# Performance work log

Hardware: AMD Instinct MI355X
Metric: run time of the kernel (lower is better)

Reference implementation:

```python
import jax, jax.numpy as jnp
import numpy as np

B, S, D_IN, D_OUT = 4, 2048, 4096, 4096
N_ADAPTERS, MAX_RANK = 8, 16


def setup_inputs() -> dict:
    key = jax.random.key(0)
    ks = jax.random.split(key, 7)
    x = jax.random.normal(ks[0], (B, S, D_IN), dtype=jnp.float32)
    weight = jax.random.normal(ks[1], (D_OUT, D_IN), dtype=jnp.float32) * (1.0 / np.sqrt(D_IN))
    bias = jax.random.normal(ks[2], (D_OUT,), dtype=jnp.float32) * 0.01
    lora_a_weights = jax.random.normal(ks[3], (N_ADAPTERS, MAX_RANK, D_IN), dtype=jnp.float32) * (1.0 / np.sqrt(D_IN))
    lora_b_weights = jax.random.normal(ks[4], (N_ADAPTERS, D_OUT, MAX_RANK), dtype=jnp.float32) * 0.02
    scaling_factors = jax.random.uniform(ks[5], (N_ADAPTERS,), dtype=jnp.float32, minval=0.5, maxval=2.0)
    adapter_id = jax.random.randint(ks[6], (B,), 0, N_ADAPTERS, dtype=jnp.int64)
    return {
        "x": x,
        "weight": weight,
        "bias": bias,
        "lora_a_weights": lora_a_weights,
        "lora_b_weights": lora_b_weights,
        "scaling_factors": scaling_factors,
        "adapter_id": adapter_id,
    }


def reference(x, weight, bias, lora_a_weights, lora_b_weights, scaling_factors, adapter_id):
    # Base linear: [B,S,Din] @ [Dout,Din]^T + bias -> [B,S,Dout]
    base = jnp.einsum('bsi,oi->bso', x, weight) + bias
    # Per-batch adapter gather (Punica/S-LoRA style bgmv)
    a_sel = lora_a_weights[adapter_id]      # [B, R, Din]
    b_sel = lora_b_weights[adapter_id]      # [B, Dout, R]
    scale = scaling_factors[adapter_id]     # [B]
    low = jnp.einsum('bsi,bri->bsr', x, a_sel)          # [B, S, R]
    delta = jnp.einsum('bsr,bor->bso', low, b_sel)      # [B, S, Dout]
    return base + scale[:, None, None] * delta
```

## Files before the change

kernel.cpp:

```cpp
#include <hip/hip_runtime.h>
#include <hip/hip_bf16.h>

#define BATCH 4
#define SEQ   2048
#define DIN   4096
#define DOUT  4096
#define MTOT  (BATCH * SEQ)
#define RANK  16

typedef __bf16 bf8_t  __attribute__((ext_vector_type(8)));
typedef float  f4_t   __attribute__((ext_vector_type(4)));

#define GLD_LDS(g, l) \
  __builtin_amdgcn_global_load_lds((const __attribute__((address_space(1))) void*)(g), \
                                   (__attribute__((address_space(3))) void*)(l), 16, 0, 0)

__global__ __launch_bounds__(256) void conv_kernel(
    const float* __restrict__ w, __bf16* __restrict__ wb) {
  const size_t i = ((size_t)blockIdx.x * 256 + threadIdx.x) * 8;
  f4_t a = *(const f4_t*)(w + i);
  f4_t b = *(const f4_t*)(w + i + 4);
  bf8_t o;
#pragma unroll
  for (int e = 0; e < 4; ++e) { o[e] = (__bf16)a[e]; o[4 + e] = (__bf16)b[e]; }
  *(bf8_t*)(wb + i) = o;
}

__global__ __launch_bounds__(256) void lora_low_kernel(
    const __bf16* __restrict__ xb, const float* __restrict__ Aw,
    const float* __restrict__ scales, const int* __restrict__ adapter_id,
    float* __restrict__ lowS) {
  const int t    = threadIdx.x;
  const int w    = t >> 6;
  const int lane = t & 63;
  const int quad = lane >> 4;
  const int l16  = lane & 15;
  const int m0   = blockIdx.x * 64;
  const int kb   = blockIdx.y * 512;
  const int b    = adapter_id[m0 >> 11];
  const float scale = scales[b];

  const int row = m0 + w * 16 + l16;
  const __bf16* xp = xb + (size_t)row * DIN + kb + quad * 8;
  const float*  ap = Aw + ((size_t)b * RANK + l16) * DIN + kb + quad * 8;

  f4_t acc = (f4_t)0.f;
#pragma unroll 4
  for (int it = 0; it < 16; ++it) {
    const int off = it * 32;
    bf8_t af = *(const bf8_t*)(xp + off);
    f4_t v0 = *(const f4_t*)(ap + off);
    f4_t v1 = *(const f4_t*)(ap + off + 4);
    bf8_t bfr;
#pragma unroll
    for (int e = 0; e < 4; ++e) { bfr[e] = (__bf16)v0[e]; bfr[4 + e] = (__bf16)v1[e]; }
    acc = __builtin_amdgcn_mfma_f32_16x16x32_bf16(af, bfr, acc, 0, 0, 0);
  }
#pragma unroll
  for (int e = 0; e < 4; ++e)
    atomicAdd(&lowS[(size_t)(m0 + w * 16 + quad * 4 + e) * RANK + l16], acc[e] * scale);
}

#define BM 256
#define BN 256
#define BKK 32
#define NT (DIN / BKK)

__global__ __launch_bounds__(512, 2) void lora_gemm_kernel(
    const __bf16* __restrict__ x, const __bf16* __restrict__ wgt,
    const float* __restrict__ bias, const float* __restrict__ loraB,
    const int* __restrict__ adapter_id, const float* __restrict__ lowS,
    float* __restrict__ out) {
  __shared__ __bf16 lds[4][2][BM * BKK];

  const int t    = threadIdx.x;
  const int w    = t >> 6;
  const int lane = t & 63;
  const int quad = lane >> 4;
  const int l16  = lane & 15;
  const int wm   = w >> 2;
  const int wn   = w & 3;
  const int m0 = blockIdx.y * BM;
  const int n0 = blockIdx.x * BN;

  const int sr = t >> 2;
  const int sc = (t & 3) ^ ((sr >> 1) & 3);
  const __bf16* gA = x   + (size_t)(m0 + sr) * DIN + sc * 8;
  const __bf16* gB = wgt + (size_t)(n0 + sr) * DIN + sc * 8;
  const int ldst = w * 512;

  const int fc   = (quad ^ ((l16 >> 1) & 3)) * 8;
  const int aoff = (wm * 128 + l16) * BKK + fc;
  const int boff = (wn * 64  + l16) * BKK + fc;

  f4_t acc[8][4];
#pragma unroll
  for (int i = 0; i < 8; ++i)
#pragma unroll
    for (int j = 0; j < 4; ++j) acc[i][j] = (f4_t)0.f;

#define STAGE(s, k0) do {                                      \
    GLD_LDS(gA + (k0),              &lds[s][0][ldst]);         \
    GLD_LDS(gA + (k0) + 128 * DIN,  &lds[s][0][4096 + ldst]);  \
    GLD_LDS(gB + (k0),              &lds[s][1][ldst]);         \
    GLD_LDS(gB + (k0) + 128 * DIN,  &lds[s][1][4096 + ldst]);  \
  } while (0)

  auto body = [&](int s) {
    bf8_t a[8], b[4];
#pragma unroll
    for (int mf = 0; mf < 8; ++mf)
      a[mf] = *(const bf8_t*)&lds[s][0][aoff + mf * (16 * BKK)];
#pragma unroll
    for (int nf = 0; nf < 4; ++nf)
      b[nf] = *(const bf8_t*)&lds[s][1][boff + nf * (16 * BKK)];
    __builtin_amdgcn_s_setprio(1);
#pragma unroll
    for (int mf = 0; mf < 8; ++mf)
#pragma unroll
      for (int nf = 0; nf < 4; ++nf)
        acc[mf][nf] = __builtin_amdgcn_mfma_f32_16x16x32_bf16(a[mf], b[nf], acc[mf][nf], 0, 0, 0);
    __builtin_amdgcn_s_setprio(0);
  };

  STAGE(0, 0); STAGE(1, BKK); STAGE(2, 2 * BKK);
  for (int it = 0; it < NT - 3; ++it) {
    STAGE((it + 3) & 3, (it + 3) * BKK);
    asm volatile("s_waitcnt vmcnt(12)" ::: "memory");
    __builtin_amdgcn_s_barrier();
    body(it & 3);
    __builtin_amdgcn_s_barrier();
  }
  asm volatile("s_waitcnt vmcnt(8)" ::: "memory");
  __builtin_amdgcn_s_barrier();
  body((NT - 3) & 3);
  __builtin_amdgcn_s_barrier();
  asm volatile("s_waitcnt vmcnt(4)" ::: "memory");
  __builtin_amdgcn_s_barrier();
  body((NT - 2) & 3);
  __builtin_amdgcn_s_barrier();
  asm volatile("s_waitcnt vmcnt(0)" ::: "memory");
  __builtin_amdgcn_s_barrier();
  body((NT - 1) & 3);
#undef STAGE

  const int b = adapter_id[m0 >> 11];
  bf8_t alow[8], blow[4];
  if (quad < 2) {
#pragma unroll
    for (int mf = 0; mf < 8; ++mf) {
      const float* p = &lowS[(size_t)(m0 + wm * 128 + mf * 16 + l16) * RANK + quad * 8];
      f4_t u0 = *(const f4_t*)p;
      f4_t u1 = *(const f4_t*)(p + 4);
#pragma unroll
      for (int e = 0; e < 4; ++e) { alow[mf][e] = (__bf16)u0[e]; alow[mf][4 + e] = (__bf16)u1[e]; }
    }
#pragma unroll
    for (int nf = 0; nf < 4; ++nf) {
      const float* p = &loraB[((size_t)b * DOUT + n0 + wn * 64 + nf * 16 + l16) * RANK + quad * 8];
      f4_t u0 = *(const f4_t*)p;
      f4_t u1 = *(const f4_t*)(p + 4);
#pragma unroll
      for (int e = 0; e < 4; ++e) { blow[nf][e] = (__bf16)u0[e]; blow[nf][4 + e] = (__bf16)u1[e]; }
    }
  } else {
#pragma unroll
    for (int i = 0; i < 8; ++i)
#pragma unroll
      for (int e = 0; e < 8; ++e) alow[i][e] = (__bf16)0.f;
#pragma unroll
    for (int j = 0; j < 4; ++j)
#pragma unroll
      for (int e = 0; e < 8; ++e) blow[j][e] = (__bf16)0.f;
  }
#pragma unroll
  for (int mf = 0; mf < 8; ++mf)
#pragma unroll
    for (int nf = 0; nf < 4; ++nf)
      acc[mf][nf] = __builtin_amdgcn_mfma_f32_16x16x32_bf16(alow[mf], blow[nf], acc[mf][nf], 0, 0, 0);

#pragma unroll
  for (int nf = 0; nf < 4; ++nf) {
    const int c = n0 + wn * 64 + nf * 16 + l16;
    const float bc = bias[c];
#pragma unroll
    for (int mf = 0; mf < 8; ++mf) {
      const int r0 = m0 + wm * 128 + mf * 16 + quad * 4;
#pragma unroll
      for (int e = 0; e < 4; ++e)
        out[(size_t)(r0 + e) * DOUT + c] = acc[mf][nf][e] + bc;
    }
  }
}

extern "C" void kernel_launch(void* const* d_in, const int* in_sizes, int n_in,
                              void* d_out, int out_size, void* d_ws, size_t ws_size,
                              hipStream_t stream) {
  const float* x       = (const float*)d_in[0];
  const float* weight  = (const float*)d_in[1];
  const float* bias    = (const float*)d_in[2];
  const float* lora_a  = (const float*)d_in[3];
  const float* lora_b  = (const float*)d_in[4];
  const float* scaling = (const float*)d_in[5];
  const int*   adapter = (const int*)d_in[6];
  float* out = (float*)d_out;

  __bf16* xb   = (__bf16*)d_ws;
  __bf16* wb   = xb + (size_t)MTOT * DIN;
  float*  lowS = (float*)(wb + (size_t)DOUT * DIN);

  hipMemsetAsync(lowS, 0, (size_t)MTOT * RANK * sizeof(float), stream);
  conv_kernel<<<(size_t)DOUT * DIN / 8 / 256, 256, 0, stream>>>(weight, wb);
  conv_kernel<<<(size_t)MTOT * DIN / 8 / 256, 256, 0, stream>>>(x, xb);
  dim3 lgrid(MTOT / 64, 8);
  lora_low_kernel<<<lgrid, 256, 0, stream>>>(xb, lora_a, scaling, adapter, lowS);
  dim3 grid(DOUT / BN, MTOT / BM);
  lora_gemm_kernel<<<grid, 512, 0, stream>>>(xb, wb, bias, lora_b, adapter, lowS, out);
}
```

Baseline: 557.4 us.

## Fuse x conversion into LoRA-down kernel and restructure GEMM pipeline with BK=64

```diff
diff --git a/kernel.cpp b/kernel.cpp
--- a/kernel.cpp
+++ b/kernel.cpp
@@ -15,7 +15,7 @@
   __builtin_amdgcn_global_load_lds((const __attribute__((address_space(1))) void*)(g), \
                                    (__attribute__((address_space(3))) void*)(l), 16, 0, 0)
 
-__global__ __launch_bounds__(256) void conv_kernel(
+__global__ __launch_bounds__(256) void conv_w_kernel(
     const float* __restrict__ w, __bf16* __restrict__ wb) {
   const size_t i = ((size_t)blockIdx.x * 256 + threadIdx.x) * 8;
   f4_t a = *(const f4_t*)(w + i);
@@ -27,9 +27,9 @@
 }
 
 __global__ __launch_bounds__(256) void lora_low_kernel(
-    const __bf16* __restrict__ xb, const float* __restrict__ Aw,
+    const float* __restrict__ x, const float* __restrict__ Aw,
     const float* __restrict__ scales, const int* __restrict__ adapter_id,
-    float* __restrict__ lowS) {
+    __bf16* __restrict__ xb, float* __restrict__ lowS) {
   const int t    = threadIdx.x;
   const int w    = t >> 6;
   const int lane = t & 63;
@@ -41,19 +41,25 @@
   const float scale = scales[b];
 
   const int row = m0 + w * 16 + l16;
-  const __bf16* xp = xb + (size_t)row * DIN + kb + quad * 8;
-  const float*  ap = Aw + ((size_t)b * RANK + l16) * DIN + kb + quad * 8;
+  const float*  xp  = x  + (size_t)row * DIN + kb + quad * 8;
+  __bf16*       xbp = xb + (size_t)row * DIN + kb + quad * 8;
+  const float*  ap  = Aw + ((size_t)b * RANK + l16) * DIN + kb + quad * 8;
 
   f4_t acc = (f4_t)0.f;
 #pragma unroll 4
   for (int it = 0; it < 16; ++it) {
     const int off = it * 32;
-    bf8_t af = *(const bf8_t*)(xp + off);
+    f4_t u0 = *(const f4_t*)(xp + off);
+    f4_t u1 = *(const f4_t*)(xp + off + 4);
     f4_t v0 = *(const f4_t*)(ap + off);
     f4_t v1 = *(const f4_t*)(ap + off + 4);
-    bf8_t bfr;
-#pragma unroll
-    for (int e = 0; e < 4; ++e) { bfr[e] = (__bf16)v0[e]; bfr[4 + e] = (__bf16)v1[e]; }
+    bf8_t af, bfr;
+#pragma unroll
+    for (int e = 0; e < 4; ++e) {
+      af[e] = (__bf16)u0[e]; af[4 + e] = (__bf16)u1[e];
+      bfr[e] = (__bf16)v0[e]; bfr[4 + e] = (__bf16)v1[e];
+    }
+    *(bf8_t*)(xbp + off) = af;
     acc = __builtin_amdgcn_mfma_f32_16x16x32_bf16(af, bfr, acc, 0, 0, 0);
   }
 #pragma unroll
@@ -63,15 +69,19 @@
 
 #define BM 256
 #define BN 256
-#define BKK 32
-#define NT (DIN / BKK)
+#define BKT 64
+#define NT (DIN / BKT)
+#define NIT (NT / 2)
+
+#define BAR() __builtin_amdgcn_s_barrier()
+#define VMW(n) asm volatile("s_waitcnt vmcnt(" #n ")" ::: "memory")
 
 __global__ __launch_bounds__(512, 2) void lora_gemm_kernel(
     const __bf16* __restrict__ x, const __bf16* __restrict__ wgt,
     const float* __restrict__ bias, const float* __restrict__ loraB,
     const int* __restrict__ adapter_id, const float* __restrict__ lowS,
     float* __restrict__ out) {
-  __shared__ __bf16 lds[4][2][BM * BKK];
+  __shared__ __bf16 lds[2][2][2][128 * 64];
 
   const int t    = threadIdx.x;
   const int w    = t >> 6;
@@ -80,71 +90,103 @@
   const int l16  = lane & 15;
   const int wm   = w >> 2;
   const int wn   = w & 3;
-  const int m0 = blockIdx.y * BM;
-  const int n0 = blockIdx.x * BN;
-
-  const int sr = t >> 2;
-  const int sc = (t & 3) ^ ((sr >> 1) & 3);
-  const __bf16* gA = x   + (size_t)(m0 + sr) * DIN + sc * 8;
-  const __bf16* gB = wgt + (size_t)(n0 + sr) * DIN + sc * 8;
-  const int ldst = w * 512;
-
-  const int fc   = (quad ^ ((l16 >> 1) & 3)) * 8;
-  const int aoff = (wm * 128 + l16) * BKK + fc;
-  const int boff = (wn * 64  + l16) * BKK + fc;
-
+
+  const int linear = blockIdx.y * 16 + blockIdx.x;
+  const int swz = (linear & 7) * 64 + (linear >> 3);
+  const int m0 = (swz >> 4) * BM;
+  const int n0 = (swz & 15) * BN;
+
+  const int srow = t >> 3;
+  const int sc   = (t & 7) ^ ((t >> 4) & 7);
+  const __bf16* gA = x   + (size_t)(m0 + srow) * DIN + sc * 8;
+  const __bf16* gB = wgt + (size_t)(n0 + srow) * DIN + sc * 8;
+  const int ldsw = w * 512;
+
+#define STG(buf, mat, half, kel, gp) do {                                        \
+    GLD_LDS((gp) + (size_t)((half) * 128) * DIN + (kel),                         \
+            &lds[buf][mat][half][ldsw]);                                         \
+    GLD_LDS((gp) + (size_t)((half) * 128 + 64) * DIN + (kel),                    \
+            &lds[buf][mat][half][4096 + ldsw]);                                  \
+  } while (0)
+
+  const int st0 = (quad ^ ((l16 >> 1) & 7)) * 8;
+  const int st1 = ((4 + quad) ^ ((l16 >> 1) & 7)) * 8;
+
+  bf8_t a[4][2], b[2][2];
   f4_t acc[8][4];
 #pragma unroll
   for (int i = 0; i < 8; ++i)
 #pragma unroll
     for (int j = 0; j < 4; ++j) acc[i][j] = (f4_t)0.f;
 
-#define STAGE(s, k0) do {                                      \
-    GLD_LDS(gA + (k0),              &lds[s][0][ldst]);         \
-    GLD_LDS(gA + (k0) + 128 * DIN,  &lds[s][0][4096 + ldst]);  \
-    GLD_LDS(gB + (k0),              &lds[s][1][ldst]);         \
-    GLD_LDS(gB + (k0) + 128 * DIN,  &lds[s][1][4096 + ldst]);  \
-  } while (0)
-
-  auto body = [&](int s) {
-    bf8_t a[8], b[4];
-#pragma unroll
-    for (int mf = 0; mf < 8; ++mf)
-      a[mf] = *(const bf8_t*)&lds[s][0][aoff + mf * (16 * BKK)];
-#pragma unroll
-    for (int nf = 0; nf < 4; ++nf)
-      b[nf] = *(const bf8_t*)&lds[s][1][boff + nf * (16 * BKK)];
-    __builtin_amdgcn_s_setprio(1);
-#pragma unroll
-    for (int mf = 0; mf < 8; ++mf)
-#pragma unroll
-      for (int nf = 0; nf < 4; ++nf)
-        acc[mf][nf] = __builtin_amdgcn_mfma_f32_16x16x32_bf16(a[mf], b[nf], acc[mf][nf], 0, 0, 0);
-    __builtin_amdgcn_s_setprio(0);
-  };
-
-  STAGE(0, 0); STAGE(1, BKK); STAGE(2, 2 * BKK);
-  for (int it = 0; it < NT - 3; ++it) {
-    STAGE((it + 3) & 3, (it + 3) * BKK);
-    asm volatile("s_waitcnt vmcnt(12)" ::: "memory");
-    __builtin_amdgcn_s_barrier();
-    body(it & 3);
-    __builtin_amdgcn_s_barrier();
-  }
-  asm volatile("s_waitcnt vmcnt(8)" ::: "memory");
-  __builtin_amdgcn_s_barrier();
-  body((NT - 3) & 3);
-  __builtin_amdgcn_s_barrier();
-  asm volatile("s_waitcnt vmcnt(4)" ::: "memory");
-  __builtin_amdgcn_s_barrier();
-  body((NT - 2) & 3);
-  __builtin_amdgcn_s_barrier();
-  asm volatile("s_waitcnt vmcnt(0)" ::: "memory");
-  __builtin_amdgcn_s_barrier();
-  body((NT - 1) & 3);
-#undef STAGE
-
-  const int b = adapter_id[m0 >> 11];
+#define LDA(buf, mh) do {                                                        \
+    const __bf16* base_ = &lds[buf][0][wm][0];                                   \
+    _Pragma("unroll")                                                            \
+    for (int mq = 0; mq < 4; ++mq) {                                             \
+      const int r_ = ((mh) * 4 + mq) * 16 + l16;                                 \
+      a[mq][0] = *(const bf8_t*)(base_ + r_ * 64 + st0);                         \
+      a[mq][1] = *(const bf8_t*)(base_ + r_ * 64 + st1);                         \
+    }                                                                            \
+  } while (0)
+
+#define LDB(buf, nh) do {                                                        \
+    const __bf16* base_ = &lds[buf][1][wn >> 1][(wn & 1) * 4096];                \
+    _Pragma("unroll")                                                            \
+    for (int nq = 0; nq < 2; ++nq) {                                             \
+      const int r_ = ((nh) * 2 + nq) * 16 + l16;                                 \
+      b[nq][0] = *(const bf8_t*)(base_ + r_ * 64 + st0);                         \
+      b[nq][1] = *(const bf8_t*)(base_ + r_ * 64 + st1);                         \
+    }                                                                            \
+  } while (0)
+
+#define MM(mh, nh) do {                                                          \
+    __builtin_amdgcn_s_setprio(1);                                               \
+    _Pragma("unroll")                                                            \
+    for (int ks = 0; ks < 2; ++ks)                                               \
+      _Pragma("unroll")                                                          \
+      for (int mq = 0; mq < 4; ++mq)                                             \
+        _Pragma("unroll")                                                        \
+        for (int nq = 0; nq < 2; ++nq)                                           \
+          acc[(mh) * 4 + mq][(nh) * 2 + nq] = __builtin_amdgcn_mfma_f32_16x16x32_bf16( \
+              a[mq][ks], b[nq][ks], acc[(mh) * 4 + mq][(nh) * 2 + nq], 0, 0, 0); \
+    __builtin_amdgcn_s_setprio(0);                                               \
+  } while (0)
+
+  STG(0, 0, 0, 0, gA); STG(0, 0, 1, 0, gA);
+  STG(0, 1, 0, 0, gB); STG(0, 1, 1, 0, gB);
+  STG(1, 0, 0, BKT, gA); STG(1, 1, 1, BKT, gB);
+  VMW(4);
+  BAR();
+
+  for (int it = 0; it < NIT; ++it) {
+    const int k1 = (2 * it + 1) * BKT;
+    const int k2 = ((2 * it + 2) & (NT - 1)) * BKT;
+    const int k3 = ((2 * it + 3) & (NT - 1)) * BKT;
+    LDA(0, 0); LDB(0, 0); STG(1, 1, 0, k1, gB);
+    BAR(); MM(0, 0); BAR();
+    LDB(0, 1); STG(1, 0, 1, k1, gA);
+    BAR(); MM(0, 1); BAR();
+    LDA(0, 1); STG(0, 0, 0, k2, gA);
+    BAR(); MM(1, 1); BAR();
+    LDB(0, 0); STG(0, 1, 1, k2, gB);
+    VMW(4);
+    BAR(); MM(1, 0); BAR();
+    LDA(1, 0); LDB(1, 0); STG(0, 1, 0, k2, gB);
+    BAR(); MM(0, 0); BAR();
+    LDB(1, 1); STG(0, 0, 1, k2, gA);
+    BAR(); MM(0, 1); BAR();
+    LDA(1, 1); STG(1, 0, 0, k3, gA);
+    BAR(); MM(1, 1); BAR();
+    LDB(1, 0); STG(1, 1, 1, k3, gB);
+    VMW(4);
+    BAR(); MM(1, 0); BAR();
+  }
+#undef STG
+#undef LDA
+#undef LDB
+#undef MM
+
+  const int b_id = adapter_id[m0 >> 11];
   bf8_t alow[8], blow[4];
   if (quad < 2) {
 #pragma unroll
@@ -157,7 +199,7 @@
     }
 #pragma unroll
     for (int nf = 0; nf < 4; ++nf) {
-      const float* p = &loraB[((size_t)b * DOUT + n0 + wn * 64 + nf * 16 + l16) * RANK + quad * 8];
+      const float* p = &loraB[((size_t)b_id * DOUT + n0 + wn * 64 + nf * 16 + l16) * RANK + quad * 8];
       f4_t u0 = *(const f4_t*)p;
       f4_t u1 = *(const f4_t*)(p + 4);
 #pragma unroll
@@ -210,10 +252,9 @@
   float*  lowS = (float*)(wb + (size_t)DOUT * DIN);
 
   hipMemsetAsync(lowS, 0, (size_t)MTOT * RANK * sizeof(float), stream);
-  conv_kernel<<<(size_t)DOUT * DIN / 8 / 256, 256, 0, stream>>>(weight, wb);
-  conv_kernel<<<(size_t)MTOT * DIN / 8 / 256, 256, 0, stream>>>(x, xb);
+  conv_w_kernel<<<(size_t)DOUT * DIN / 8 / 256, 256, 0, stream>>>(weight, wb);
   dim3 lgrid(MTOT / 64, 8);
-  lora_low_kernel<<<lgrid, 256, 0, stream>>>(xb, lora_a, scaling, adapter, lowS);
+  lora_low_kernel<<<lgrid, 256, 0, stream>>>(x, lora_a, scaling, adapter, xb, lowS);
   dim3 grid(DOUT / BN, MTOT / BM);
   lora_gemm_kernel<<<grid, 512, 0, stream>>>(xb, wb, bias, lora_b, adapter, lowS, out);
 }
```

Measured after the change: 504.0 us. 9.6% less time.
